# Kernel optimization log

Hardware: AMD Instinct MI355X
Metric: run time of the kernel (lower is better)

Reference implementation:

```python
import jax, jax.numpy as jnp
import numpy as np

NSAMPLE = 1024   # FPS centroids S
NGROUP = 32      # neighbors per ball K
RADIUS = 0.2


def _sqdist(a, b):
    # a: [B,S,3], b: [B,N,3] -> [B,S,N] squared euclidean distances
    return (jnp.sum(a * a, -1)[:, :, None]
            + jnp.sum(b * b, -1)[:, None, :]
            - 2.0 * jnp.einsum('bsc,bnc->bsn', a, b))


def farthest_point_sample(xyz, npoint):
    # xyz: [B,N,3] -> indices [B,npoint]. Deterministic start at index 0
    # (torch version randomizes the first centroid).
    B, N, _ = xyz.shape

    def step(carry, _):
        distance, farthest = carry
        centroid = jnp.take_along_axis(xyz, farthest[:, None, None], axis=1)  # [B,1,3]
        d = jnp.sum((xyz - centroid) ** 2, -1)                                 # [B,N]
        distance = jnp.minimum(distance, d)
        new_far = jnp.argmax(distance, -1).astype(jnp.int32)
        return (distance, new_far), farthest

    init = (jnp.full((B, N), 1e10, xyz.dtype), jnp.zeros((B,), jnp.int32))
    _, cents = jax.lax.scan(step, init, None, length=npoint)  # [npoint,B]
    return cents.T  # [B,npoint]


def query_ball_point(radius, nsample, xyz, new_xyz):
    # xyz: [B,N,3], new_xyz: [B,S,3] -> int idx [B,S,nsample]
    B, N, _ = xyz.shape
    sqr = _sqdist(new_xyz, xyz)                       # [B,S,N]
    idx = jnp.broadcast_to(jnp.arange(N, dtype=jnp.int32), sqr.shape)
    idx = jnp.where(sqr > radius * radius, N, idx)    # invalid -> sentinel N
    idx = jnp.sort(idx, axis=-1)[:, :, :nsample]      # smallest valid indices first
    first = idx[:, :, :1]
    idx = jnp.where(idx == N, first, idx)             # pad with first neighbor
    return idx.astype(jnp.int32)


def _gather_points(points, idx):
    # points: [B,N,C], idx: [B,S,K] -> [B,S,K,C]
    return jax.vmap(lambda p, i: p[i])(points, idx)


def setup_inputs() -> dict:
    key = jax.random.key(0)
    ks = jax.random.split(key, 8)
    B, N, D = 16, 8192, 64
    xyz = jax.random.uniform(ks[0], (B, N, 3), dtype=jnp.float32)
    points_fea = jax.random.normal(ks[1], (B, N, D), dtype=jnp.float32)
    s = 0.05
    W1 = jax.random.normal(ks[2], (67, 64), dtype=jnp.float32) * s
    b1 = jnp.zeros((64,), jnp.float32)
    W2 = jax.random.normal(ks[3], (64, 128), dtype=jnp.float32) * s
    b2 = jnp.zeros((128,), jnp.float32)
    W3 = jax.random.normal(ks[4], (128, 256), dtype=jnp.float32) * s
    b3 = jnp.zeros((256,), jnp.float32)
    return {"xyz": xyz, "points_fea": points_fea, "W1": W1, "b1": b1,
            "W2": W2, "b2": b2, "W3": W3, "b3": b3}


def reference(xyz, points_fea, W1, b1, W2, b2, W3, b3):
    # --- sample_and_group (fps + ball query) ---
    fps_idx = farthest_point_sample(xyz, NSAMPLE)                       # [B,S]
    sampled_xyz = jnp.take_along_axis(xyz, fps_idx[..., None], axis=1)  # [B,S,3]
    grouped_idx = query_ball_point(RADIUS, NGROUP, xyz, sampled_xyz)    # [B,S,K]
    grouped_xyz = _gather_points(xyz, grouped_idx)                      # [B,S,K,3]
    rel = grouped_xyz - sampled_xyz[:, :, None, :]
    grouped_fea = _gather_points(points_fea, grouped_idx)               # [B,S,K,D]
    feats = jnp.concatenate([rel, grouped_fea], axis=-1)                # [B,S,K,3+D]
    # --- per-point MLP (Linear+ReLU x3) ---
    h = jax.nn.relu(feats @ W1 + b1)
    h = jax.nn.relu(h @ W2 + b2)
    h = jax.nn.relu(h @ W3 + b3)                                        # [B,S,K,256]
    # --- max-pool over neighbors ---
    out = jnp.max(h, axis=2)                                            # [B,S,256]
    return sampled_xyz, out
```

## Files before the change

kernel.cpp:

```cpp
#include <hip/hip_runtime.h>
#include <hip/hip_bf16.h>

#define N_PTS 8192
#define NSAMP 1024
#define NGRP  32

typedef __attribute__((ext_vector_type(8))) short bf16x8;
typedef __attribute__((ext_vector_type(4))) float f32x4;
typedef __attribute__((ext_vector_type(2))) float f32x2;

static __device__ inline unsigned short f2bf(float f) {
  __hip_bfloat16 h = __float2bfloat16(f);
  return __builtin_bit_cast(unsigned short, h);
}

#define DPP_MAXSTEP(r, ctrl)                                                  \
  r = fmaxf(r, __int_as_float(__builtin_amdgcn_update_dpp(                    \
          __float_as_int(r), __float_as_int(r), (ctrl), 0xf, 0xf, false)))

#define FINAL8(P, V, F) do {                                                  \
    const uint4* pp_ = (const uint4*)&(P)[0];                                 \
    uint4 p0_ = pp_[0], p1_ = pp_[1], p2_ = pp_[2], p3_ = pp_[3];             \
    V = __uint_as_float(p0_.x); F = p0_.y;                                    \
    float q_;                                                                 \
    q_ = __uint_as_float(p0_.z); if (q_ > V) { V = q_; F = p0_.w; }           \
    q_ = __uint_as_float(p1_.x); if (q_ > V) { V = q_; F = p1_.y; }           \
    q_ = __uint_as_float(p1_.z); if (q_ > V) { V = q_; F = p1_.w; }           \
    q_ = __uint_as_float(p2_.x); if (q_ > V) { V = q_; F = p2_.y; }           \
    q_ = __uint_as_float(p2_.z); if (q_ > V) { V = q_; F = p2_.w; }           \
    q_ = __uint_as_float(p3_.x); if (q_ > V) { V = q_; F = p3_.y; }           \
    q_ = __uint_as_float(p3_.z); if (q_ > V) { V = q_; F = p3_.w; }           \
  } while (0)

static __device__ inline void load16(const float* __restrict__ bx, int t,
                                     float px[16], float py[16], float pz[16]) {
  const float4* src = (const float4*)(bx + t * 48);
  float4 v0 = src[0], v1 = src[1], v2 = src[2];
  float4 v3 = src[3], v4 = src[4], v5 = src[5];
  float4 v6 = src[6], v7 = src[7], v8 = src[8];
  float4 v9 = src[9], v10 = src[10], v11 = src[11];
  px[ 0]=v0.x; py[ 0]=v0.y; pz[ 0]=v0.z;
  px[ 1]=v0.w; py[ 1]=v1.x; pz[ 1]=v1.y;
  px[ 2]=v1.z; py[ 2]=v1.w; pz[ 2]=v2.x;
  px[ 3]=v2.y; py[ 3]=v2.z; pz[ 3]=v2.w;
  px[ 4]=v3.x; py[ 4]=v3.y; pz[ 4]=v3.z;
  px[ 5]=v3.w; py[ 5]=v4.x; pz[ 5]=v4.y;
  px[ 6]=v4.z; py[ 6]=v4.w; pz[ 6]=v5.x;
  px[ 7]=v5.y; py[ 7]=v5.z; pz[ 7]=v5.w;
  px[ 8]=v6.x; py[ 8]=v6.y; pz[ 8]=v6.z;
  px[ 9]=v6.w; py[ 9]=v7.x; pz[ 9]=v7.y;
  px[10]=v7.z; py[10]=v7.w; pz[10]=v8.x;
  px[11]=v8.y; py[11]=v8.z; pz[11]=v8.w;
  px[12]=v9.x; py[12]=v9.y; pz[12]=v9.z;
  px[13]=v9.w; py[13]=v10.x; pz[13]=v10.y;
  px[14]=v10.z; py[14]=v10.w; pz[14]=v11.x;
  px[15]=v11.y; py[15]=v11.z; pz[15]=v11.w;
}

__global__
__attribute__((amdgpu_flat_work_group_size(512, 512)))
__attribute__((amdgpu_waves_per_eu(2, 2)))
void fps_kernel(
    const float* __restrict__ xyz, float* __restrict__ out_sampled)
{
  #pragma clang fp contract(off)
  const int b = blockIdx.x;
  const int t = threadIdx.x;
  const float* bx = xyz + (size_t)b * N_PTS * 3;

  float px[16], py[16], pz[16];
  load16(bx, t, px, py, pz);

  f32x2 px2[8], py2[8], pz2[8], ds2[8];
  #pragma unroll
  for (int j = 0; j < 8; ++j) {
    px2[j] = (f32x2){px[2*j], px[2*j+1]};
    py2[j] = (f32x2){py[2*j], py[2*j+1]};
    pz2[j] = (f32x2){pz[2*j], pz[2*j+1]};
    ds2[j] = (f32x2){10000000000.0f, 10000000000.0f};
  }

  __shared__ float lds_p[N_PTS * 3];
  __shared__ float out_lds[NSAMP * 3];
  __shared__ __align__(16) uint2 part[2][8];

  for (int i = t; i < N_PTS * 3; i += 512) lds_p[i] = bx[i];

  const int lane = t & 63;
  const int wv   = t >> 6;

  float cx = bx[0], cy = bx[1], cz = bx[2];

  for (int it = 0; it < NSAMP; ++it) {
    if (t == 0) {
      out_lds[it * 3 + 0] = cx;
      out_lds[it * 3 + 1] = cy;
      out_lds[it * 3 + 2] = cz;
    }

    const f32x2 c2x = (f32x2){cx, cx};
    const f32x2 c2y = (f32x2){cy, cy};
    const f32x2 c2z = (f32x2){cz, cz};
    f32x2 bv2 = (f32x2){-1.0f, -1.0f};
    #pragma unroll
    for (int j = 0; j < 8; ++j) {
      f32x2 dx = px2[j] - c2x;
      f32x2 dy = py2[j] - c2y;
      f32x2 dz = pz2[j] - c2z;
      f32x2 d  = __builtin_elementwise_fma(
          dz, dz, __builtin_elementwise_fma(dy, dy, dx * dx));
      f32x2 nd = __builtin_elementwise_min(ds2[j], d);
      ds2[j] = nd;
      bv2 = __builtin_elementwise_max(bv2, nd);
    }
    float bv = fmaxf(bv2.x, bv2.y);

    int bi = t * 16 + 15;
    #pragma unroll
    for (int r = 14; r >= 0; --r) {
      float dr = (r & 1) ? ds2[r >> 1].y : ds2[r >> 1].x;
      bi = (dr == bv) ? (t * 16 + r) : bi;
    }

    float rmax = bv;
    DPP_MAXSTEP(rmax, 0x111);
    DPP_MAXSTEP(rmax, 0x112);
    DPP_MAXSTEP(rmax, 0x114);
    DPP_MAXSTEP(rmax, 0x118);
    DPP_MAXSTEP(rmax, 0x142);
    DPP_MAXSTEP(rmax, 0x143);
    float vmax = __int_as_float(
        __builtin_amdgcn_readlane(__float_as_int(rmax), 63));

    unsigned long long m = __ballot(bv == vmax);
    int L = __ffsll((long long)m) - 1;
    int widx = __builtin_amdgcn_readlane(bi, L);

    const int slot = it & 1;
    if (lane == 0) part[slot][wv] = make_uint2(__float_as_uint(vmax), (unsigned)widx);
    __syncthreads();

    float v; unsigned f;
    FINAL8(part[slot], v, f);

    cx = lds_p[f * 3 + 0];
    cy = lds_p[f * 3 + 1];
    cz = lds_p[f * 3 + 2];
  }

  __syncthreads();
  float* ob = out_sampled + (size_t)b * NSAMP * 3;
  for (int i = t; i < NSAMP * 3; i += 512) ob[i] = out_lds[i];
}

__global__ __launch_bounds__(256) void ball_kernel(
    const float* __restrict__ xyz, const float* __restrict__ sampled,
    int* __restrict__ gidx)
{
  #pragma clang fp contract(off)
  const float R2 = (float)(0.2 * 0.2);
  int gt = blockIdx.x * 256 + threadIdx.x;
  int w = gt >> 6;
  int lane = gt & 63;
  const int b = w >> 10;
  const float* cp = sampled + (size_t)w * 3;
  float cx = cp[0], cy = cp[1], cz = cp[2];
  float na = ((cx * cx) + (cy * cy)) + (cz * cz);
  const float* bx = xyz + (size_t)b * N_PTS * 3;
  int* out = gidx + (size_t)w * NGRP;

  int cnt = 0;
  int first = 0;
  for (int base = 0; base < N_PTS && cnt < NGRP; base += 64) {
    int p = base + lane;
    float x = bx[p * 3 + 0];
    float y = bx[p * 3 + 1];
    float z = bx[p * 3 + 2];
    float nb  = ((x * x) + (y * y)) + (z * z);
    float dot = fmaf(cz, z, fmaf(cy, y, cx * x));
    float sq  = (na + nb) - (2.0f * dot);
    bool inr = !(sq > R2);
    unsigned long long m = __ballot(inr);
    if (cnt == 0 && m != 0ull) first = base + (__ffsll(m) - 1);
    int before = __popcll(m & ((1ull << lane) - 1ull));
    int pos = cnt + before;
    if (inr && pos < NGRP) out[pos] = p;
    cnt += __popcll(m);
  }
  if (cnt < NGRP) {
    int q = cnt + lane;
    if (q < NGRP) out[q] = first;
  }
}

__global__ __launch_bounds__(256) void prep_w_kernel(
    const float* __restrict__ W1, const float* __restrict__ W2,
    const float* __restrict__ W3, unsigned short* __restrict__ wf1,
    unsigned short* __restrict__ wf2, unsigned short* __restrict__ wf3)
{
  int tid = blockIdx.x * 256 + threadIdx.x;
  int rec = tid >> 6, lane = tid & 63;
  if (rec >= 92) return;
  const float* W; unsigned short* dst; int N, K, ksteps, rl; int permuted;
  if (rec < 12)      { W = W1; dst = wf1; N = 64;  K = 67;  ksteps = 3; rl = rec;     permuted = 1; }
  else if (rec < 28) { W = W2; dst = wf2; N = 128; K = 64;  ksteps = 2; rl = rec - 12; permuted = 0; }
  else               { W = W3; dst = wf3; N = 256; K = 128; ksteps = 4; rl = rec - 28; permuted = 0; }
  int nt = rl / ksteps, ks = rl - nt * ksteps;
  int n  = nt * 16 + (lane & 15);
  int kb = ks * 32 + (lane >> 4) * 8;
  unsigned short v[8] __attribute__((aligned(16)));
  #pragma unroll
  for (int j = 0; j < 8; ++j) {
    int k = kb + j;
    float val;
    if (permuted) {
      if (k < 64)      val = W[(k + 3) * N + n];
      else if (k < K)  val = W[(k - 64) * N + n];
      else             val = 0.0f;
    } else {
      val = (k < K) ? W[k * N + n] : 0.0f;
    }
    v[j] = f2bf(val);
  }
  *(uint4*)(dst + ((size_t)rl * 64 + lane) * 8) = *(const uint4*)v;
}

__global__ __launch_bounds__(256, 4) void mlp_mfma_kernel(
    const float* __restrict__ xyz, const float* __restrict__ fea,
    const float* __restrict__ sampled, const int* __restrict__ gidx,
    const unsigned short* __restrict__ wf1, const unsigned short* __restrict__ wf2,
    const unsigned short* __restrict__ wf3, const float* __restrict__ b1,
    const float* __restrict__ b2, const float* __restrict__ b3,
    float* __restrict__ out)
{
  __shared__ __align__(16) unsigned short fT[64][104];
  __shared__ __align__(16) unsigned short h1[64][72];
  __shared__ __align__(16) unsigned short h2[64][136];
  __shared__ int   sidx[64];
  __shared__ float sc[8];

  const int wk  = (blockIdx.x & 7) * 1024 + (blockIdx.x >> 3);
  const int bs0 = wk * 2;
  const int b   = bs0 >> 10;
  const int t   = threadIdx.x;
  const int w    = t >> 6;
  const int lane = t & 63;
  const int quad = lane >> 4;
  const int ncol = lane & 15;

  if (t < 64) sidx[t] = gidx[(size_t)bs0 * 32 + t];
  if (t < 6)  sc[t] = sampled[(size_t)bs0 * 3 + t];
  __syncthreads();

  {
    const int pt = t >> 2, c0 = t & 3;
    const int p = sidx[pt];
    const float4* fp4 = (const float4*)(fea + ((size_t)b * N_PTS + p) * 64);
    #pragma unroll
    for (int j = 0; j < 4; ++j) {
      float4 fv = fp4[c0 + 4 * j];
      unsigned short s4[4] __attribute__((aligned(8)));
      s4[0] = f2bf(fv.x); s4[1] = f2bf(fv.y);
      s4[2] = f2bf(fv.z); s4[3] = f2bf(fv.w);
      *(uint2*)&fT[pt][(c0 + 4 * j) * 4] = *(const uint2*)s4;
    }
    if (c0 == 0) {
      const float* xp = xyz + ((size_t)b * N_PTS + p) * 3;
      const int cc = (pt >> 5) * 3;
      unsigned short sr[4] __attribute__((aligned(8)));
      sr[0] = f2bf(xp[0] - sc[cc + 0]);
      sr[1] = f2bf(xp[1] - sc[cc + 1]);
      sr[2] = f2bf(xp[2] - sc[cc + 2]);
      sr[3] = 0;
      *(uint2*)&fT[pt][64] = *(const uint2*)sr;
      *(uint2*)&fT[pt][68] = (uint2){0u, 0u};
    } else {
      *(uint4*)&fT[pt][72 + (c0 - 1) * 8] = (uint4){0u, 0u, 0u, 0u};
    }
  }
  __syncthreads();

  {
    const int nt = w;
    float bb = b1[nt * 16 + ncol];
    f32x4 acc[4];
    #pragma unroll
    for (int mt = 0; mt < 4; ++mt) acc[mt] = (f32x4){bb, bb, bb, bb};
    #pragma unroll
    for (int ks = 0; ks < 3; ++ks) {
      bf16x8 bf = *(const bf16x8*)(wf1 + ((size_t)(nt * 3 + ks) * 64 + lane) * 8);
      #pragma unroll
      for (int mt = 0; mt < 4; ++mt) {
        bf16x8 a = *(const bf16x8*)&fT[mt * 16 + ncol][ks * 32 + quad * 8];
        acc[mt] = __builtin_amdgcn_mfma_f32_16x16x32_bf16(a, bf, acc[mt], 0, 0, 0);
      }
    }
    #pragma unroll
    for (int mt = 0; mt < 4; ++mt)
      #pragma unroll
      for (int r = 0; r < 4; ++r)
        h1[mt * 16 + quad * 4 + r][nt * 16 + ncol] = f2bf(fmaxf(acc[mt][r], 0.0f));
  }
  __syncthreads();

  #pragma unroll
  for (int i = 0; i < 2; ++i) {
    const int nt = 2 * w + i;
    float bb = b2[nt * 16 + ncol];
    f32x4 acc[4];
    #pragma unroll
    for (int mt = 0; mt < 4; ++mt) acc[mt] = (f32x4){bb, bb, bb, bb};
    #pragma unroll
    for (int ks = 0; ks < 2; ++ks) {
      bf16x8 bf = *(const bf16x8*)(wf2 + ((size_t)(nt * 2 + ks) * 64 + lane) * 8);
      #pragma unroll
      for (int mt = 0; mt < 4; ++mt) {
        bf16x8 a = *(const bf16x8*)&h1[mt * 16 + ncol][ks * 32 + quad * 8];
        acc[mt] = __builtin_amdgcn_mfma_f32_16x16x32_bf16(a, bf, acc[mt], 0, 0, 0);
      }
    }
    #pragma unroll
    for (int mt = 0; mt < 4; ++mt)
      #pragma unroll
      for (int r = 0; r < 4; ++r)
        h2[mt * 16 + quad * 4 + r][nt * 16 + ncol] = f2bf(fmaxf(acc[mt][r], 0.0f));
  }
  __syncthreads();

  #pragma unroll
  for (int half = 0; half < 2; ++half) {
    f32x4 acc[2][4];
    #pragma unroll
    for (int i = 0; i < 2; ++i) {
      const int nt = 4 * w + half * 2 + i;
      float bb = b3[nt * 16 + ncol];
      #pragma unroll
      for (int mt = 0; mt < 4; ++mt) acc[i][mt] = (f32x4){bb, bb, bb, bb};
    }
    #pragma unroll
    for (int ks = 0; ks < 4; ++ks) {
      bf16x8 a[4];
      #pragma unroll
      for (int mt = 0; mt < 4; ++mt)
        a[mt] = *(const bf16x8*)&h2[mt * 16 + ncol][ks * 32 + quad * 8];
      #pragma unroll
      for (int i = 0; i < 2; ++i) {
        const int nt = 4 * w + half * 2 + i;
        bf16x8 bf = *(const bf16x8*)(wf3 + ((size_t)(nt * 4 + ks) * 64 + lane) * 8);
        #pragma unroll
        for (int mt = 0; mt < 4; ++mt)
          acc[i][mt] = __builtin_amdgcn_mfma_f32_16x16x32_bf16(a[mt], bf, acc[i][mt], 0, 0, 0);
      }
    }
    #pragma unroll
    for (int i = 0; i < 2; ++i) {
      const int nt = 4 * w + half * 2 + i;
      float m0 = fmaxf(fmaxf(acc[i][0][0], acc[i][0][1]),
                       fmaxf(acc[i][0][2], acc[i][0][3]));
      m0 = fmaxf(m0, fmaxf(fmaxf(acc[i][1][0], acc[i][1][1]),
                           fmaxf(acc[i][1][2], acc[i][1][3])));
      float m1 = fmaxf(fmaxf(acc[i][2][0], acc[i][2][1]),
                       fmaxf(acc[i][2][2], acc[i][2][3]));
      m1 = fmaxf(m1, fmaxf(fmaxf(acc[i][3][0], acc[i][3][1]),
                           fmaxf(acc[i][3][2], acc[i][3][3])));
      m0 = fmaxf(m0, __shfl_xor(m0, 16));
      m0 = fmaxf(m0, __shfl_xor(m0, 32));
      m1 = fmaxf(m1, __shfl_xor(m1, 16));
      m1 = fmaxf(m1, __shfl_xor(m1, 32));
      if (quad == 0)
        out[(size_t)bs0 * 256 + nt * 16 + ncol] = fmaxf(m0, 0.0f);
      else if (quad == 1)
        out[(size_t)(bs0 + 1) * 256 + nt * 16 + ncol] = fmaxf(m1, 0.0f);
    }
  }
}

extern "C" void kernel_launch(void* const* d_in, const int* in_sizes, int n_in,
                              void* d_out, int out_size, void* d_ws, size_t ws_size,
                              hipStream_t stream) {
  const float* xyz = (const float*)d_in[0];
  const float* fea = (const float*)d_in[1];
  const float* W1  = (const float*)d_in[2];
  const float* b1  = (const float*)d_in[3];
  const float* W2  = (const float*)d_in[4];
  const float* b2  = (const float*)d_in[5];
  const float* W3  = (const float*)d_in[6];
  const float* b3  = (const float*)d_in[7];

  float* outp    = (float*)d_out;
  float* sampled = outp;
  float* mlp_out = outp + 16 * 1024 * 3;
  int*   gidx    = (int*)d_ws;
  unsigned short* wf1 = (unsigned short*)((char*)d_ws + (2u << 20));
  unsigned short* wf2 = wf1 + (size_t)12 * 64 * 8;
  unsigned short* wf3 = wf2 + (size_t)16 * 64 * 8;

  fps_kernel<<<16, 512, 0, stream>>>(xyz, sampled);
  prep_w_kernel<<<23, 256, 0, stream>>>(W1, W2, W3, wf1, wf2, wf3);
  ball_kernel<<<4096, 256, 0, stream>>>(xyz, sampled, gidx);
  mlp_mfma_kernel<<<8192, 256, 0, stream>>>(xyz, fea, sampled, gidx,
                                            wf1, wf2, wf3, b1, b2, b3, mlp_out);
}
```

Before: 1.014 ms.

## Add SoA ball query with prefetch and double MLP tile to four centroids

Adds a prep kernel that converts xyz to padded structure-of-arrays with precomputed squared norms. A new ball-query kernel reads coalesced x/y/z/norm arrays and prefetches the next 64-point chunk, used when the workspace is large enough. Separately, the MLP kernel now processes four centroids (128 rows) per block instead of two, so each weight fragment is reused across twice as many rows. The cost is larger LDS use and more accumulator registers, with the occupancy hint lowered from 4 to 2.

```diff
diff --git a/kernel.cpp b/kernel.cpp
--- a/kernel.cpp
+++ b/kernel.cpp
@@ -4,6 +4,7 @@
 #define N_PTS 8192
 #define NSAMP 1024
 #define NGRP  32
+#define SOA_PAD 8256
 
 typedef __attribute__((ext_vector_type(8))) short bf16x8;
 typedef __attribute__((ext_vector_type(4))) float f32x4;
@@ -153,6 +154,72 @@
   for (int i = t; i < NSAMP * 3; i += 512) ob[i] = out_lds[i];
 }
 
+__global__ __launch_bounds__(256) void prep_soa_kernel(
+    const float* __restrict__ xyz, float* __restrict__ xs,
+    float* __restrict__ ys, float* __restrict__ zs, float* __restrict__ ns)
+{
+  #pragma clang fp contract(off)
+  int tid = blockIdx.x * 256 + threadIdx.x;
+  int b = tid / SOA_PAD, p = tid - b * SOA_PAD;
+  if (b >= 16) return;
+  float x = 0.0f, y = 0.0f, z = 0.0f, nb = 0.0f;
+  if (p < N_PTS) {
+    const float* q = xyz + ((size_t)b * N_PTS + p) * 3;
+    x = q[0]; y = q[1]; z = q[2];
+    nb = ((x * x) + (y * y)) + (z * z);
+  }
+  size_t o = (size_t)b * SOA_PAD + p;
+  xs[o] = x; ys[o] = y; zs[o] = z; ns[o] = nb;
+}
+
+__global__ __launch_bounds__(256) void ball_soa_kernel(
+    const float* __restrict__ xs, const float* __restrict__ ys,
+    const float* __restrict__ zs, const float* __restrict__ ns,
+    const float* __restrict__ sampled, int* __restrict__ gidx)
+{
+  #pragma clang fp contract(off)
+  const float R2 = (float)(0.2 * 0.2);
+  int gt = blockIdx.x * 256 + threadIdx.x;
+  int w = gt >> 6;
+  int lane = gt & 63;
+  const int b = w >> 10;
+  const float* cp = sampled + (size_t)w * 3;
+  float cx = cp[0], cy = cp[1], cz = cp[2];
+  float na = ((cx * cx) + (cy * cy)) + (cz * cz);
+  const float* bxs = xs + (size_t)b * SOA_PAD;
+  const float* bys = ys + (size_t)b * SOA_PAD;
+  const float* bzs = zs + (size_t)b * SOA_PAD;
+  const float* bns = ns + (size_t)b * SOA_PAD;
+  int* out = gidx + (size_t)w * NGRP;
+
+  int cnt = 0;
+  int first = 0;
+  float x = bxs[lane], y = bys[lane], z = bzs[lane], nb = bns[lane];
+  for (int base = 0; base < N_PTS && cnt < NGRP; base += 64) {
+    float xN = bxs[base + 64 + lane];
+    float yN = bys[base + 64 + lane];
+    float zN = bzs[base + 64 + lane];
+    float nN = bns[base + 64 + lane];
+
+    int p = base + lane;
+    float dot = fmaf(cz, z, fmaf(cy, y, cx * x));
+    float sq  = (na + nb) - (2.0f * dot);
+    bool inr = !(sq > R2);
+    unsigned long long m = __ballot(inr);
+    if (cnt == 0 && m != 0ull) first = base + (__ffsll(m) - 1);
+    int before = __popcll(m & ((1ull << lane) - 1ull));
+    int pos = cnt + before;
+    if (inr && pos < NGRP) out[pos] = p;
+    cnt += __popcll(m);
+
+    x = xN; y = yN; z = zN; nb = nN;
+  }
+  if (cnt < NGRP) {
+    int q = cnt + lane;
+    if (q < NGRP) out[q] = first;
+  }
+}
+
 __global__ __launch_bounds__(256) void ball_kernel(
     const float* __restrict__ xyz, const float* __restrict__ sampled,
     int* __restrict__ gidx)
@@ -225,7 +292,7 @@
   *(uint4*)(dst + ((size_t)rl * 64 + lane) * 8) = *(const uint4*)v;
 }
 
-__global__ __launch_bounds__(256, 4) void mlp_mfma_kernel(
+__global__ __launch_bounds__(256, 2) void mlp_mfma_kernel(
     const float* __restrict__ xyz, const float* __restrict__ fea,
     const float* __restrict__ sampled, const int* __restrict__ gidx,
     const unsigned short* __restrict__ wf1, const unsigned short* __restrict__ wf2,
@@ -233,14 +300,14 @@
     const float* __restrict__ b2, const float* __restrict__ b3,
     float* __restrict__ out)
 {
-  __shared__ __align__(16) unsigned short fT[64][104];
-  __shared__ __align__(16) unsigned short h1[64][72];
-  __shared__ __align__(16) unsigned short h2[64][136];
-  __shared__ int   sidx[64];
-  __shared__ float sc[8];
-
-  const int wk  = (blockIdx.x & 7) * 1024 + (blockIdx.x >> 3);
-  const int bs0 = wk * 2;
+  __shared__ __align__(16) unsigned short fT[128][104];
+  __shared__ __align__(16) unsigned short h1[128][72];
+  __shared__ __align__(16) unsigned short h2[128][136];
+  __shared__ int   sidx[128];
+  __shared__ float sc[16];
+
+  const int wk  = (blockIdx.x & 7) * 512 + (blockIdx.x >> 3);
+  const int bs0 = wk * 4;
   const int b   = bs0 >> 10;
   const int t   = threadIdx.x;
   const int w    = t >> 6;
@@ -248,21 +315,21 @@
   const int quad = lane >> 4;
   const int ncol = lane & 15;
 
-  if (t < 64) sidx[t] = gidx[(size_t)bs0 * 32 + t];
-  if (t < 6)  sc[t] = sampled[(size_t)bs0 * 3 + t];
+  if (t < 128) sidx[t] = gidx[(size_t)bs0 * 32 + t];
+  if (t < 12)  sc[t] = sampled[(size_t)bs0 * 3 + t];
   __syncthreads();
 
   {
-    const int pt = t >> 2, c0 = t & 3;
+    const int pt = t >> 1, c0 = t & 1;
     const int p = sidx[pt];
     const float4* fp4 = (const float4*)(fea + ((size_t)b * N_PTS + p) * 64);
     #pragma unroll
-    for (int j = 0; j < 4; ++j) {
-      float4 fv = fp4[c0 + 4 * j];
+    for (int j = 0; j < 8; ++j) {
+      float4 fv = fp4[c0 + 2 * j];
       unsigned short s4[4] __attribute__((aligned(8)));
       s4[0] = f2bf(fv.x); s4[1] = f2bf(fv.y);
       s4[2] = f2bf(fv.z); s4[3] = f2bf(fv.w);
-      *(uint2*)&fT[pt][(c0 + 4 * j) * 4] = *(const uint2*)s4;
+      *(uint2*)&fT[pt][(c0 + 2 * j) * 4] = *(const uint2*)s4;
     }
     if (c0 == 0) {
       const float* xp = xyz + ((size_t)b * N_PTS + p) * 3;
@@ -275,7 +342,9 @@
       *(uint2*)&fT[pt][64] = *(const uint2*)sr;
       *(uint2*)&fT[pt][68] = (uint2){0u, 0u};
     } else {
-      *(uint4*)&fT[pt][72 + (c0 - 1) * 8] = (uint4){0u, 0u, 0u, 0u};
+      *(uint4*)&fT[pt][72] = (uint4){0u, 0u, 0u, 0u};
+      *(uint4*)&fT[pt][80] = (uint4){0u, 0u, 0u, 0u};
+      *(uint4*)&fT[pt][88] = (uint4){0u, 0u, 0u, 0u};
     }
   }
   __syncthreads();
@@ -283,20 +352,20 @@
   {
     const int nt = w;
     float bb = b1[nt * 16 + ncol];
-    f32x4 acc[4];
-    #pragma unroll
-    for (int mt = 0; mt < 4; ++mt) acc[mt] = (f32x4){bb, bb, bb, bb};
+    f32x4 acc[8];
+    #pragma unroll
+    for (int mt = 0; mt < 8; ++mt) acc[mt] = (f32x4){bb, bb, bb, bb};
     #pragma unroll
     for (int ks = 0; ks < 3; ++ks) {
       bf16x8 bf = *(const bf16x8*)(wf1 + ((size_t)(nt * 3 + ks) * 64 + lane) * 8);
       #pragma unroll
-      for (int mt = 0; mt < 4; ++mt) {
+      for (int mt = 0; mt < 8; ++mt) {
         bf16x8 a = *(const bf16x8*)&fT[mt * 16 + ncol][ks * 32 + quad * 8];
         acc[mt] = __builtin_amdgcn_mfma_f32_16x16x32_bf16(a, bf, acc[mt], 0, 0, 0);
       }
     }
     #pragma unroll
-    for (int mt = 0; mt < 4; ++mt)
+    for (int mt = 0; mt < 8; ++mt)
       #pragma unroll
       for (int r = 0; r < 4; ++r)
         h1[mt * 16 + quad * 4 + r][nt * 16 + ncol] = f2bf(fmaxf(acc[mt][r], 0.0f));
@@ -307,20 +376,20 @@
   for (int i = 0; i < 2; ++i) {
     const int nt = 2 * w + i;
     float bb = b2[nt * 16 + ncol];
-    f32x4 acc[4];
-    #pragma unroll
-    for (int mt = 0; mt < 4; ++mt) acc[mt] = (f32x4){bb, bb, bb, bb};
+    f32x4 acc[8];
+    #pragma unroll
+    for (int mt = 0; mt < 8; ++mt) acc[mt] = (f32x4){bb, bb, bb, bb};
     #pragma unroll
     for (int ks = 0; ks < 2; ++ks) {
       bf16x8 bf = *(const bf16x8*)(wf2 + ((size_t)(nt * 2 + ks) * 64 + lane) * 8);
       #pragma unroll
-      for (int mt = 0; mt < 4; ++mt) {
+      for (int mt = 0; mt < 8; ++mt) {
         bf16x8 a = *(const bf16x8*)&h1[mt * 16 + ncol][ks * 32 + quad * 8];
         acc[mt] = __builtin_amdgcn_mfma_f32_16x16x32_bf16(a, bf, acc[mt], 0, 0, 0);
       }
     }
     #pragma unroll
-    for (int mt = 0; mt < 4; ++mt)
+    for (int mt = 0; mt < 8; ++mt)
       #pragma unroll
       for (int r = 0; r < 4; ++r)
         h2[mt * 16 + quad * 4 + r][nt * 16 + ncol] = f2bf(fmaxf(acc[mt][r], 0.0f));
@@ -328,50 +397,43 @@
   __syncthreads();
 
   #pragma unroll
-  for (int half = 0; half < 2; ++half) {
-    f32x4 acc[2][4];
-    #pragma unroll
-    for (int i = 0; i < 2; ++i) {
-      const int nt = 4 * w + half * 2 + i;
-      float bb = b3[nt * 16 + ncol];
-      #pragma unroll
-      for (int mt = 0; mt < 4; ++mt) acc[i][mt] = (f32x4){bb, bb, bb, bb};
-    }
+  for (int pass = 0; pass < 4; ++pass) {
+    const int nt = 4 * w + pass;
+    float bb = b3[nt * 16 + ncol];
+    f32x4 acc[8];
+    #pragma unroll
+    for (int mt = 0; mt < 8; ++mt) acc[mt] = (f32x4){bb, bb, bb, bb};
     #pragma unroll
     for (int ks = 0; ks < 4; ++ks) {
-      bf16x8 a[4];
-      #pragma unroll
-      for (int mt = 0; mt < 4; ++mt)
+      bf16x8 a[8];
+      #pragma unroll
+      for (int mt = 0; mt < 8; ++mt)
         a[mt] = *(const bf16x8*)&h2[mt * 16 + ncol][ks * 32 + quad * 8];
-      #pragma unroll
-      for (int i = 0; i < 2; ++i) {
-        const int nt = 4 * w + half * 2 + i;
-        bf16x8 bf = *(const bf16x8*)(wf3 + ((size_t)(nt * 4 + ks) * 64 + lane) * 8);
-        #pragma unroll
-        for (int mt = 0; mt < 4; ++mt)
-          acc[i][mt] = __builtin_amdgcn_mfma_f32_16x16x32_bf16(a[mt], bf, acc[i][mt], 0, 0, 0);
-      }
-    }
-    #pragma unroll
-    for (int i = 0; i < 2; ++i) {
-      const int nt = 4 * w + half * 2 + i;
-      float m0 = fmaxf(fmaxf(acc[i][0][0], acc[i][0][1]),
-                       fmaxf(acc[i][0][2], acc[i][0][3]));
-      m0 = fmaxf(m0, fmaxf(fmaxf(acc[i][1][0], acc[i][1][1]),
-                           fmaxf(acc[i][1][2], acc[i][1][3])));
-      float m1 = fmaxf(fmaxf(acc[i][2][0], acc[i][2][1]),
-                       fmaxf(acc[i][2][2], acc[i][2][3]));
-      m1 = fmaxf(m1, fmaxf(fmaxf(acc[i][3][0], acc[i][3][1]),
-                           fmaxf(acc[i][3][2], acc[i][3][3])));
-      m0 = fmaxf(m0, __shfl_xor(m0, 16));
-      m0 = fmaxf(m0, __shfl_xor(m0, 32));
-      m1 = fmaxf(m1, __shfl_xor(m1, 16));
-      m1 = fmaxf(m1, __shfl_xor(m1, 32));
-      if (quad == 0)
-        out[(size_t)bs0 * 256 + nt * 16 + ncol] = fmaxf(m0, 0.0f);
-      else if (quad == 1)
-        out[(size_t)(bs0 + 1) * 256 + nt * 16 + ncol] = fmaxf(m1, 0.0f);
-    }
+      bf16x8 bf = *(const bf16x8*)(wf3 + ((size_t)(nt * 4 + ks) * 64 + lane) * 8);
+      #pragma unroll
+      for (int mt = 0; mt < 8; ++mt)
+        acc[mt] = __builtin_amdgcn_mfma_f32_16x16x32_bf16(a[mt], bf, acc[mt], 0, 0, 0);
+    }
+    float m0 = fmaxf(fmaxf(fmaxf(acc[0][0], acc[0][1]), fmaxf(acc[0][2], acc[0][3])),
+                     fmaxf(fmaxf(acc[1][0], acc[1][1]), fmaxf(acc[1][2], acc[1][3])));
+    float m1 = fmaxf(fmaxf(fmaxf(acc[2][0], acc[2][1]), fmaxf(acc[2][2], acc[2][3])),
+                     fmaxf(fmaxf(acc[3][0], acc[3][1]), fmaxf(acc[3][2], acc[3][3])));
+    float m2 = fmaxf(fmaxf(fmaxf(acc[4][0], acc[4][1]), fmaxf(acc[4][2], acc[4][3])),
+                     fmaxf(fmaxf(acc[5][0], acc[5][1]), fmaxf(acc[5][2], acc[5][3])));
+    float m3 = fmaxf(fmaxf(fmaxf(acc[6][0], acc[6][1]), fmaxf(acc[6][2], acc[6][3])),
+                     fmaxf(fmaxf(acc[7][0], acc[7][1]), fmaxf(acc[7][2], acc[7][3])));
+    m0 = fmaxf(m0, __shfl_xor(m0, 16)); m0 = fmaxf(m0, __shfl_xor(m0, 32));
+    m1 = fmaxf(m1, __shfl_xor(m1, 16)); m1 = fmaxf(m1, __shfl_xor(m1, 32));
+    m2 = fmaxf(m2, __shfl_xor(m2, 16)); m2 = fmaxf(m2, __shfl_xor(m2, 32));
+    m3 = fmaxf(m3, __shfl_xor(m3, 16)); m3 = fmaxf(m3, __shfl_xor(m3, 32));
+    if (quad == 0)
+      out[(size_t)bs0 * 256 + nt * 16 + ncol] = fmaxf(m0, 0.0f);
+    else if (quad == 1)
+      out[(size_t)(bs0 + 1) * 256 + nt * 16 + ncol] = fmaxf(m1, 0.0f);
+    else if (quad == 2)
+      out[(size_t)(bs0 + 2) * 256 + nt * 16 + ncol] = fmaxf(m2, 0.0f);
+    else
+      out[(size_t)(bs0 + 3) * 256 + nt * 16 + ncol] = fmaxf(m3, 0.0f);
   }
 }
 
@@ -394,10 +456,21 @@
   unsigned short* wf1 = (unsigned short*)((char*)d_ws + (2u << 20));
   unsigned short* wf2 = wf1 + (size_t)12 * 64 * 8;
   unsigned short* wf3 = wf2 + (size_t)16 * 64 * 8;
+  float* xs = (float*)((char*)d_ws + (2u << 20) + (96u << 10));
+  float* ys = xs + (size_t)16 * SOA_PAD;
+  float* zs = ys + (size_t)16 * SOA_PAD;
+  float* ns = zs + (size_t)16 * SOA_PAD;
+  const size_t soa_need = (2u << 20) + (96u << 10) +
+                          4ull * 16 * SOA_PAD * sizeof(float);
 
   fps_kernel<<<16, 512, 0, stream>>>(xyz, sampled);
   prep_w_kernel<<<23, 256, 0, stream>>>(W1, W2, W3, wf1, wf2, wf3);
-  ball_kernel<<<4096, 256, 0, stream>>>(xyz, sampled, gidx);
-  mlp_mfma_kernel<<<8192, 256, 0, stream>>>(xyz, fea, sampled, gidx,
+  if (ws_size >= soa_need) {
+    prep_soa_kernel<<<516, 256, 0, stream>>>(xyz, xs, ys, zs, ns);
+    ball_soa_kernel<<<4096, 256, 0, stream>>>(xs, ys, zs, ns, sampled, gidx);
+  } else {
+    ball_kernel<<<4096, 256, 0, stream>>>(xyz, sampled, gidx);
+  }
+  mlp_mfma_kernel<<<4096, 256, 0, stream>>>(xyz, fea, sampled, gidx,
                                             wf1, wf2, wf3, b1, b2, b3, mlp_out);
 }
```

Result: slower. 1.035 ms (+2.0%).
